# Optimization experiments

Hardware: AMD Instinct MI355X
Metric: run time of the kernel (lower is better)

## Reference

```python
import jax, jax.numpy as jnp
import numpy as np

EPS = 1e-08

def _masked_stats(x, m, denom):
    # x: [B,C,H,W] already multiplied by mask; m: [B,1,H,W]; denom: [B,1,1,1]
    mean = jnp.sum(x, axis=(2, 3), keepdims=True) / denom          # [B,C,1,1]
    var = jnp.sum(((x - mean) * m) ** 2, axis=(2, 3), keepdims=True) / denom
    return mean, jnp.maximum(var, 0.0)

def _modulate(w, a, b):
    # concat [B,C,1,1]+[B,C,1,1] -> [B,2C], linear (no bias), back to [B,C,1,1]
    v = jnp.concatenate([a, b], axis=1)[:, :, 0, 0]                # [B,2C]
    y = v @ w.T                                                    # [B,C]
    return y[:, :, None, None]

def setup_inputs() -> dict:
    key = jax.random.key(0)
    ks = jax.random.split(key, 7)
    B, C, H, W = 4, 128, 256, 256
    x1 = jax.random.normal(ks[0], (B, C, H, W), dtype=jnp.float32)
    x2 = jax.random.normal(ks[1], (B, C, H, W), dtype=jnp.float32)
    mask = jax.random.uniform(ks[2], (B, 1, H // 2, W // 2), dtype=jnp.float32)
    w_in_mean = jax.random.normal(ks[3], (C, 2 * C), dtype=jnp.float32) * 0.05
    w_in_var = jax.random.normal(ks[4], (C, 2 * C), dtype=jnp.float32) * 0.05
    w_out_mean = jax.random.normal(ks[5], (C, 2 * C), dtype=jnp.float32) * 0.05
    w_out_var = jax.random.normal(ks[6], (C, 2 * C), dtype=jnp.float32) * 0.05
    return {"x1": x1, "x2": x2, "mask": mask,
            "w_in_mean": w_in_mean, "w_in_var": w_in_var,
            "w_out_mean": w_out_mean, "w_out_var": w_out_var}

def reference(x1, x2, mask, w_in_mean, w_in_var, w_out_mean, w_out_var):
    H, W = x1.shape[2], x1.shape[3]
    # nearest-neighbor upsample of mask to x1 spatial size (integer factor)
    rh, rw = H // mask.shape[2], W // mask.shape[3]
    m = jnp.repeat(jnp.repeat(mask, rh, axis=2), rw, axis=3)       # [B,1,H,W]
    om = 1.0 - m
    n_in = jnp.sum(m, axis=(2, 3), keepdims=True) + EPS            # [B,1,1,1]
    n_out = jnp.sum(om, axis=(2, 3), keepdims=True) + EPS

    x1_in, x2_in = x1 * m, x2 * m
    x1_out, x2_out = x1 * om, x2 * om

    x1_in_mean, x1_in_var = _masked_stats(x1_in, m, n_in)
    x2_in_mean, x2_in_var = _masked_stats(x2_in, m, n_in)
    x1_out_mean, x1_out_var = _masked_stats(x1_out, om, n_out)
    x2_out_mean, x2_out_var = _masked_stats(x2_out, om, n_out)

    ada_in_mean = _modulate(w_in_mean, x1_in_mean, x2_in_mean)
    ada_in_var = _modulate(w_in_var, x1_in_var, x2_in_var)
    ada_out_mean = _modulate(w_out_mean, x1_out_mean, x2_out_mean)
    ada_out_var = _modulate(w_out_var, x1_out_var, x2_out_var)

    norm_in = (x1_in - x1_in_mean) * jax.lax.rsqrt(x1_in_var + EPS)
    norm_out = (x1_out - x1_out_mean) * jax.lax.rsqrt(x1_out_var + EPS)
    ada_x1_in = norm_in * ada_in_var + ada_in_mean
    ada_x1_out = norm_out * ada_out_var + ada_out_mean
    return ada_x1_in * m + ada_x1_out * om
```

## Files before the change

### kernel.cpp

```cpp
#include <hip/hip_runtime.h>

#define EPS 1e-8f

using f32x4 = __attribute__((ext_vector_type(4))) float;

__global__ __launch_bounds__(256) void k_stats(
    const float* __restrict__ x1,
    const float* __restrict__ x2,
    const float* __restrict__ mask,
    float* __restrict__ stats)
{
    int blk = blockIdx.x;
    int s   = blk & 3;
    int bc  = blk >> 2;
    int b   = bc >> 7;
    int tid = threadIdx.x;

    const float* xp1 = x1 + (size_t)bc * 65536 + s * 16384;
    const float* xp2 = x2 + (size_t)bc * 65536 + s * 16384;
    const float* mp  = mask + b * 16384;

    float a[12];
#pragma unroll
    for (int j = 0; j < 12; ++j) a[j] = 0.f;

    int base0 = s * 16384;
    for (int it = 0; it < 8; ++it) {
        int off = it * 2048 + tid * 8;
        int gi  = base0 + off;
        int h = gi >> 8;
        int w = gi & 255;
        const f32x4 v1a = *(const f32x4*)(xp1 + off);
        const f32x4 v1b = *(const f32x4*)(xp1 + off + 4);
        const f32x4 v2a = *(const f32x4*)(xp2 + off);
        const f32x4 v2b = *(const f32x4*)(xp2 + off + 4);
        const f32x4 mv  = *(const f32x4*)(mp + (h >> 1) * 128 + (w >> 1));
#pragma unroll
        for (int j = 0; j < 8; ++j) {
            float m  = mv[j >> 1];
            float om = 1.f - m;
            float m2 = m * m, om2 = om * om;
            float f1 = (j < 4) ? v1a[j & 3] : v1b[j & 3];
            float f2 = (j < 4) ? v2a[j & 3] : v2b[j & 3];
            float p1 = f1 * m2,  p2 = f2 * m2;
            a[0] += f1 * m;  a[1] += p1 * m;  a[2] += p1 * p1;
            a[3] += f2 * m;  a[4] += p2 * m;  a[5] += p2 * p2;
            float q1 = f1 * om2, q2 = f2 * om2;
            a[6] += f1 * om; a[7] += q1 * om; a[8] += q1 * q1;
            a[9] += f2 * om; a[10]+= q2 * om; a[11]+= q2 * q2;
        }
    }
#pragma unroll
    for (int j = 0; j < 12; ++j)
#pragma unroll
        for (int d = 32; d > 0; d >>= 1)
            a[j] += __shfl_down(a[j], d, 64);

    __shared__ float red[4][12];
    int wv = tid >> 6, ln = tid & 63;
    if (ln == 0) {
#pragma unroll
        for (int j = 0; j < 12; ++j) red[wv][j] = a[j];
    }
    __syncthreads();
    if (tid < 12) {
        float v = red[0][tid] + red[1][tid] + red[2][tid] + red[3][tid];
        stats[(size_t)blk * 12 + tid] = v;
    }
}

__global__ __launch_bounds__(256) void k_mod(
    const float* __restrict__ mask,
    const float* __restrict__ w_in_mean,
    const float* __restrict__ w_in_var,
    const float* __restrict__ w_out_mean,
    const float* __restrict__ w_out_var,
    const float* __restrict__ stats,
    float* __restrict__ derived)
{
    int b   = blockIdx.x;
    int tid = threadIdx.x;

    const float* mp = mask + b * 16384;
    float sm = 0.f, sm2 = 0.f;
    for (int it = 0; it < 16; ++it) {
        const f32x4 mv = *(const f32x4*)(mp + (it * 256 + tid) * 4);
#pragma unroll
        for (int j = 0; j < 4; ++j) { float m = mv[j]; sm += m; sm2 += m * m; }
    }
#pragma unroll
    for (int d = 32; d > 0; d >>= 1) {
        sm  += __shfl_down(sm, d, 64);
        sm2 += __shfl_down(sm2, d, 64);
    }
    __shared__ float rr[8];
    __shared__ float SMs, SM2s;
    int wv = tid >> 6, ln = tid & 63;
    if (ln == 0) { rr[wv] = sm; rr[4 + wv] = sm2; }
    __syncthreads();
    if (tid == 0) {
        SMs  = 4.f * (rr[0] + rr[1] + rr[2] + rr[3]);
        SM2s = 4.f * (rr[4] + rr[5] + rr[6] + rr[7]);
    }
    __syncthreads();
    float SM = SMs, SM2 = SM2s;
    float n_in  = SM + EPS;
    float n_out = 65536.f - SM + EPS;
    float SOM2  = 65536.f - 2.f * SM + SM2;

    __shared__ float vin_mean[256], vin_var[256], vout_mean[256], vout_var[256];

    if (tid < 128) {
        int c = tid;
        const float* st = stats + (size_t)(b * 128 + c) * 4 * 12;
        float s[12];
#pragma unroll
        for (int j = 0; j < 12; ++j) s[j] = st[j] + st[12 + j] + st[24 + j] + st[36 + j];
        float mi1 = s[0] / n_in;
        float vi1 = fmaxf((s[2] - 2.f * mi1 * s[1] + mi1 * mi1 * SM2) / n_in, 0.f);
        float mi2 = s[3] / n_in;
        float vi2 = fmaxf((s[5] - 2.f * mi2 * s[4] + mi2 * mi2 * SM2) / n_in, 0.f);
        float mo1 = s[6] / n_out;
        float vo1 = fmaxf((s[8] - 2.f * mo1 * s[7] + mo1 * mo1 * SOM2) / n_out, 0.f);
        float mo2 = s[9] / n_out;
        float vo2 = fmaxf((s[11] - 2.f * mo2 * s[10] + mo2 * mo2 * SOM2) / n_out, 0.f);
        vin_mean[c] = mi1;  vin_mean[128 + c] = mi2;
        vin_var[c]  = vi1;  vin_var[128 + c]  = vi2;
        vout_mean[c] = mo1; vout_mean[128 + c] = mo2;
        vout_var[c]  = vo1; vout_var[128 + c]  = vo2;
        float* d = derived + (size_t)(b * 128 + c) * 8;
        d[0] = mi1; d[1] = rsqrtf(vi1 + EPS);
        d[2] = mo1; d[3] = rsqrtf(vo1 + EPS);
    }
    __syncthreads();

    for (int t = tid; t < 512; t += 256) {
        int mat = t >> 7, row = t & 127;
        const float* wp;
        const float* vec;
        if (mat == 0)      { wp = w_in_mean;  vec = vin_mean; }
        else if (mat == 1) { wp = w_in_var;   vec = vin_var; }
        else if (mat == 2) { wp = w_out_mean; vec = vout_mean; }
        else               { wp = w_out_var;  vec = vout_var; }
        wp += row * 256;
        float acc = 0.f;
        for (int k = 0; k < 256; k += 4) {
            f32x4 wv4 = *(const f32x4*)(wp + k);
#pragma unroll
            for (int j = 0; j < 4; ++j) acc += wv4[j] * vec[k + j];
        }
        derived[(size_t)(b * 128 + row) * 8 + 4 + mat] = acc;
    }
}

__global__ __launch_bounds__(256) void k_apply(
    const float* __restrict__ x1,
    const float* __restrict__ mask,
    const float* __restrict__ derived,
    float* __restrict__ out)
{
    int blk   = blockIdx.x;
    int bc    = blk >> 5;
    int chunk = blk & 31;
    int b     = bc >> 7;
    const float* d = derived + (size_t)bc * 8;
    float mean_in = d[0], inv_in = d[1], mean_out = d[2], inv_out = d[3];
    float am_in = d[4], av_in = d[5], am_out = d[6], av_out = d[7];
    float ci1 = inv_in * av_in;
    float ci0 = am_in - mean_in * ci1;
    float co1 = inv_out * av_out;
    float co0 = am_out - mean_out * co1;

    int tid = threadIdx.x;
    int off = chunk * 2048 + tid * 8;
    int h = off >> 8, w = off & 255;
    const f32x4 xa = *(const f32x4*)(x1 + (size_t)bc * 65536 + off);
    const f32x4 xb = *(const f32x4*)(x1 + (size_t)bc * 65536 + off + 4);
    const f32x4 mv = *(const f32x4*)(mask + b * 16384 + (h >> 1) * 128 + (w >> 1));
    f32x4 oa, ob;
#pragma unroll
    for (int j = 0; j < 8; ++j) {
        float m  = mv[j >> 1];
        float om = 1.f - m;
        float x  = (j < 4) ? xa[j & 3] : xb[j & 3];
        float r  = x * (m * m * ci1 + om * om * co1) + ci0 * m + co0 * om;
        if (j < 4) oa[j & 3] = r; else ob[j & 3] = r;
    }
    *(f32x4*)(out + (size_t)bc * 65536 + off)     = oa;
    *(f32x4*)(out + (size_t)bc * 65536 + off + 4) = ob;
}

extern "C" void kernel_launch(void* const* d_in, const int* in_sizes, int n_in,
                              void* d_out, int out_size, void* d_ws, size_t ws_size,
                              hipStream_t stream) {
    const float* x1        = (const float*)d_in[0];
    const float* x2        = (const float*)d_in[1];
    const float* mask      = (const float*)d_in[2];
    const float* w_in_mean = (const float*)d_in[3];
    const float* w_in_var  = (const float*)d_in[4];
    const float* w_out_mean= (const float*)d_in[5];
    const float* w_out_var = (const float*)d_in[6];

    float* stats   = (float*)d_ws;
    float* derived = stats + 2048 * 12;
    float* out = (float*)d_out;

    k_stats<<<4 * 128 * 4, 256, 0, stream>>>(x1, x2, mask, stats);
    k_mod<<<4, 256, 0, stream>>>(mask, w_in_mean, w_in_var, w_out_mean, w_out_var,
                                 stats, derived);
    k_apply<<<4 * 128 * 32, 256, 0, stream>>>(x1, mask, derived, out);
}
```

Before: 375.3 us.

## Software-pipeline loads in stats and apply kernels with fewer, larger blocks

The stats kernel now uses 2 blocks per channel plane instead of 4 and double-buffers its global loads, prefetching the next tile while reducing the current one. The apply kernel switches from one tile per block to 8 tiles per block with the same register prefetch, uses nontemporal stores for the output, and amortises the per-channel coefficient setup. The intent is to hide memory latency and cut block-launch overhead in this bandwidth-bound workload. In exchange there are fewer blocks, which may reduce occupancy and wave-level parallelism on a GPU with many CUs, and higher register pressure.

```diff
diff --git a/kernel.cpp b/kernel.cpp
--- a/kernel.cpp
+++ b/kernel.cpp
@@ -11,37 +11,48 @@
     float* __restrict__ stats)
 {
     int blk = blockIdx.x;
-    int s   = blk & 3;
-    int bc  = blk >> 2;
+    int s   = blk & 1;
+    int bc  = blk >> 1;
     int b   = bc >> 7;
     int tid = threadIdx.x;
 
-    const float* xp1 = x1 + (size_t)bc * 65536 + s * 16384;
-    const float* xp2 = x2 + (size_t)bc * 65536 + s * 16384;
+    const size_t poff = (size_t)bc * 65536 + (size_t)s * 32768;
+    const float* xp1 = x1 + poff;
+    const float* xp2 = x2 + poff;
     const float* mp  = mask + b * 16384;
+    const int gi0 = s * 32768 + tid * 8;
 
     float a[12];
 #pragma unroll
     for (int j = 0; j < 12; ++j) a[j] = 0.f;
 
-    int base0 = s * 16384;
-    for (int it = 0; it < 8; ++it) {
-        int off = it * 2048 + tid * 8;
-        int gi  = base0 + off;
-        int h = gi >> 8;
-        int w = gi & 255;
-        const f32x4 v1a = *(const f32x4*)(xp1 + off);
-        const f32x4 v1b = *(const f32x4*)(xp1 + off + 4);
-        const f32x4 v2a = *(const f32x4*)(xp2 + off);
-        const f32x4 v2b = *(const f32x4*)(xp2 + off + 4);
-        const f32x4 mv  = *(const f32x4*)(mp + (h >> 1) * 128 + (w >> 1));
+    int off0 = tid * 8;
+    f32x4 c1a = *(const f32x4*)(xp1 + off0);
+    f32x4 c1b = *(const f32x4*)(xp1 + off0 + 4);
+    f32x4 c2a = *(const f32x4*)(xp2 + off0);
+    f32x4 c2b = *(const f32x4*)(xp2 + off0 + 4);
+    int h0 = gi0 >> 8, w0 = gi0 & 255;
+    f32x4 cm = *(const f32x4*)(mp + (h0 >> 1) * 128 + (w0 >> 1));
+
+    for (int g = 0; g < 16; ++g) {
+        f32x4 n1a, n1b, n2a, n2b, nm;
+        if (g < 15) {
+            int off = (g + 1) * 2048 + tid * 8;
+            int gi  = gi0 + (g + 1) * 2048;
+            int h = gi >> 8, w = gi & 255;
+            n1a = *(const f32x4*)(xp1 + off);
+            n1b = *(const f32x4*)(xp1 + off + 4);
+            n2a = *(const f32x4*)(xp2 + off);
+            n2b = *(const f32x4*)(xp2 + off + 4);
+            nm  = *(const f32x4*)(mp + (h >> 1) * 128 + (w >> 1));
+        }
 #pragma unroll
         for (int j = 0; j < 8; ++j) {
-            float m  = mv[j >> 1];
+            float m  = cm[j >> 1];
             float om = 1.f - m;
             float m2 = m * m, om2 = om * om;
-            float f1 = (j < 4) ? v1a[j & 3] : v1b[j & 3];
-            float f2 = (j < 4) ? v2a[j & 3] : v2b[j & 3];
+            float f1 = (j < 4) ? c1a[j & 3] : c1b[j & 3];
+            float f2 = (j < 4) ? c2a[j & 3] : c2b[j & 3];
             float p1 = f1 * m2,  p2 = f2 * m2;
             a[0] += f1 * m;  a[1] += p1 * m;  a[2] += p1 * p1;
             a[3] += f2 * m;  a[4] += p2 * m;  a[5] += p2 * p2;
@@ -49,7 +60,9 @@
             a[6] += f1 * om; a[7] += q1 * om; a[8] += q1 * q1;
             a[9] += f2 * om; a[10]+= q2 * om; a[11]+= q2 * q2;
         }
-    }
+        c1a = n1a; c1b = n1b; c2a = n2a; c2b = n2b; cm = nm;
+    }
+
 #pragma unroll
     for (int j = 0; j < 12; ++j)
 #pragma unroll
@@ -112,10 +125,10 @@
 
     if (tid < 128) {
         int c = tid;
-        const float* st = stats + (size_t)(b * 128 + c) * 4 * 12;
+        const float* st = stats + (size_t)(b * 128 + c) * 2 * 12;
         float s[12];
 #pragma unroll
-        for (int j = 0; j < 12; ++j) s[j] = st[j] + st[12 + j] + st[24 + j] + st[36 + j];
+        for (int j = 0; j < 12; ++j) s[j] = st[j] + st[12 + j];
         float mi1 = s[0] / n_in;
         float vi1 = fmaxf((s[2] - 2.f * mi1 * s[1] + mi1 * mi1 * SM2) / n_in, 0.f);
         float mi2 = s[3] / n_in;
@@ -160,8 +173,8 @@
     float* __restrict__ out)
 {
     int blk   = blockIdx.x;
-    int bc    = blk >> 5;
-    int chunk = blk & 31;
+    int bc    = blk >> 2;
+    int chunk = blk & 3;
     int b     = bc >> 7;
     const float* d = derived + (size_t)bc * 8;
     float mean_in = d[0], inv_in = d[1], mean_out = d[2], inv_out = d[3];
@@ -172,22 +185,39 @@
     float co0 = am_out - mean_out * co1;
 
     int tid = threadIdx.x;
-    int off = chunk * 2048 + tid * 8;
-    int h = off >> 8, w = off & 255;
-    const f32x4 xa = *(const f32x4*)(x1 + (size_t)bc * 65536 + off);
-    const f32x4 xb = *(const f32x4*)(x1 + (size_t)bc * 65536 + off + 4);
-    const f32x4 mv = *(const f32x4*)(mask + b * 16384 + (h >> 1) * 128 + (w >> 1));
-    f32x4 oa, ob;
-#pragma unroll
-    for (int j = 0; j < 8; ++j) {
-        float m  = mv[j >> 1];
-        float om = 1.f - m;
-        float x  = (j < 4) ? xa[j & 3] : xb[j & 3];
-        float r  = x * (m * m * ci1 + om * om * co1) + ci0 * m + co0 * om;
-        if (j < 4) oa[j & 3] = r; else ob[j & 3] = r;
-    }
-    *(f32x4*)(out + (size_t)bc * 65536 + off)     = oa;
-    *(f32x4*)(out + (size_t)bc * 65536 + off + 4) = ob;
+    const float* xp = x1 + (size_t)bc * 65536;
+    float* op = out + (size_t)bc * 65536;
+    const float* mp = mask + b * 16384;
+    const int gi0 = chunk * 16384 + tid * 8;
+
+    f32x4 cxa = *(const f32x4*)(xp + gi0);
+    f32x4 cxb = *(const f32x4*)(xp + gi0 + 4);
+    int h0 = gi0 >> 8, w0 = gi0 & 255;
+    f32x4 cm = *(const f32x4*)(mp + (h0 >> 1) * 128 + (w0 >> 1));
+
+    for (int g = 0; g < 8; ++g) {
+        f32x4 nxa, nxb, nm;
+        if (g < 7) {
+            int gi = gi0 + (g + 1) * 2048;
+            int h = gi >> 8, w = gi & 255;
+            nxa = *(const f32x4*)(xp + gi);
+            nxb = *(const f32x4*)(xp + gi + 4);
+            nm  = *(const f32x4*)(mp + (h >> 1) * 128 + (w >> 1));
+        }
+        f32x4 oa, ob;
+#pragma unroll
+        for (int j = 0; j < 8; ++j) {
+            float m  = cm[j >> 1];
+            float om = 1.f - m;
+            float x  = (j < 4) ? cxa[j & 3] : cxb[j & 3];
+            float r  = x * (m * m * ci1 + om * om * co1) + ci0 * m + co0 * om;
+            if (j < 4) oa[j & 3] = r; else ob[j & 3] = r;
+        }
+        int go = gi0 + g * 2048;
+        __builtin_nontemporal_store(oa, (f32x4*)(op + go));
+        __builtin_nontemporal_store(ob, (f32x4*)(op + go + 4));
+        cxa = nxa; cxb = nxb; cm = nm;
+    }
 }
 
 extern "C" void kernel_launch(void* const* d_in, const int* in_sizes, int n_in,
@@ -202,11 +232,11 @@
     const float* w_out_var = (const float*)d_in[6];
 
     float* stats   = (float*)d_ws;
-    float* derived = stats + 2048 * 12;
+    float* derived = stats + 1024 * 12;
     float* out = (float*)d_out;
 
-    k_stats<<<4 * 128 * 4, 256, 0, stream>>>(x1, x2, mask, stats);
+    k_stats<<<512 * 2, 256, 0, stream>>>(x1, x2, mask, stats);
     k_mod<<<4, 256, 0, stream>>>(mask, w_in_mean, w_in_var, w_out_mean, w_out_var,
                                  stats, derived);
-    k_apply<<<4 * 128 * 32, 256, 0, stream>>>(x1, mask, derived, out);
-}
+    k_apply<<<512 * 4, 256, 0, stream>>>(x1, mask, derived, out);
+}
```

Measured after the change: 374.6 us. Within noise of the previous version (-0.2%).
